# Kernel optimization log

Hardware: AMD Instinct MI355X
Metric: run time of the kernel (lower is better)

## Reference

```python
import math
import jax, jax.numpy as jnp
import numpy as np
from jax import lax

B, S, D = 2, 1024, 768
H, E, DH = 12, 8, 64          # n_head, num_experts, head dim
KA = 1                        # top-k experts per head (attention)
KF = 2                        # top-k experts per token (FFN)
DFF = 2048
EMA_DECAY = 0.99
CAP_FACTOR = 1.25
NEG_INF = -1e9


def setup_inputs() -> dict:
    key = jax.random.key(0)
    ks = jax.random.split(key, 16)
    sc = 0.02
    x = jax.random.normal(ks[0], (B, S, D), jnp.float32)
    causal = jnp.tril(jnp.ones((S, S), jnp.float32))
    mask = jnp.where(causal > 0, 0.0, NEG_INF).astype(jnp.float32)
    return {
        "x": x,
        "mask": mask,
        "W_q": jax.random.normal(ks[1], (D, D), jnp.float32) * sc,
        "W_k": jax.random.normal(ks[2], (D, D), jnp.float32) * sc,
        "W_v": jax.random.normal(ks[3], (H, E, DH, DH), jnp.float32) * sc,
        "W_o": jax.random.normal(ks[4], (H, E, DH, DH), jnp.float32) * sc,
        "W_router": jax.random.normal(ks[5], (D, H * E), jnp.float32) * sc,
        "g1": jnp.ones((D,), jnp.float32),
        "b1": jnp.zeros((D,), jnp.float32),
        "g2": jnp.ones((D,), jnp.float32),
        "b2": jnp.zeros((D,), jnp.float32),
        "gate_ff": jax.random.normal(ks[6], (D, E), jnp.float32) * sc,
        "W1": jax.random.normal(ks[7], (E, D, DFF), jnp.float32) * sc,
        "W2": jax.random.normal(ks[8], (E, DFF, D), jnp.float32) * sc,
    }


def layer_norm(x, g, b, eps=1e-5):
    m = jnp.mean(x, -1, keepdims=True)
    v = jnp.var(x, -1, keepdims=True)
    return (x - m) * lax.rsqrt(v + eps) * g + b


def head_switch_attention(x, mask, W_q, W_k, W_v, W_o, W_router):
    b, s, d = x.shape
    q = (x @ W_q).reshape(b, s, H, DH)
    k = (x @ W_k).reshape(b, s, H, DH)
    scores = jnp.einsum("bshd,bthd->bhst", q, k) / math.sqrt(DH) + mask
    p_attn = jax.nn.softmax(scores, axis=-1)          # (B,H,S,S)
    gate_logits = (x @ W_router).reshape(b, s, H, E)
    topk_scores, topk_idx = lax.top_k(gate_logits, KA)  # (B,S,H,KA)
    probs = jax.nn.softmax(topk_scores, axis=-1)
    x_h = x.reshape(b, s, H, DH)
    # value projections for all experts (small d_h x d_h GEMMs)
    v_all = jnp.einsum("bshd,hedf->bshef", x_h, W_v)
    y = jnp.zeros_like(x_h)
    hard_counts = jnp.zeros((H, E), jnp.float32)
    for slot in range(KA):
        oh = jax.nn.one_hot(topk_idx[..., slot], E, dtype=x.dtype)  # (B,S,H,E)
        v_sel = jnp.einsum("bshef,bshe->bshf", v_all, oh)
        # faithful to original einsum 'bhst,hbsd->hbtd' (sums over s)
        attn_out = jnp.einsum("bhst,bshf->bthf", p_attn, v_sel)
        o_all = jnp.einsum("bthf,hefg->btheg", attn_out, W_o)
        o_sel = jnp.einsum("btheg,bthe->bthg", o_all, oh)
        y = y + o_sel * probs[..., slot][..., None]
        hard_counts = hard_counts + lax.stop_gradient(oh).sum((0, 1))
    y = y.reshape(b, s, d)
    # EMA buffers start at zero -> ema = (1-decay)*hard/denom
    ema = hard_counts / (b * s * KA) * (1.0 - EMA_DECAY)
    p_lb = ema / (ema.sum() + 1e-9)
    aux = (p_lb * p_lb).sum() * E * H
    return y, aux


def moe_ffn(x, gate_ff, W1, W2):
    b, s, d = x.shape
    gate_logits = x @ gate_ff                      # (B,S,E), eval: no noise
    topk_scores, topk_idx = lax.top_k(gate_logits, KF)
    probs = jax.nn.softmax(topk_scores, axis=-1)   # (B,S,KF)
    capacity = math.ceil(CAP_FACTOR * (b * s) / E)
    flat_idx = topk_idx.reshape(-1)                # (B*S*KF,)
    oh_flat = jax.nn.one_hot(flat_idx, E, dtype=jnp.float32)
    tokens_so_far = jnp.cumsum(oh_flat, axis=0)
    keep = jnp.take_along_axis(tokens_so_far <= capacity, flat_idx[:, None], axis=1)[:, 0]
    probs = probs * keep.reshape(b, s, KF).astype(probs.dtype)
    probs = probs / (probs.sum(-1, keepdims=True) + 1e-9)
    oh = jax.nn.one_hot(topk_idx, E, dtype=probs.dtype)   # (B,S,KF,E)
    w = (probs[..., None] * oh).sum(2).reshape(b * s, E)  # combined weight per (token, expert)
    xf = x.reshape(b * s, d)
    yf = jnp.zeros_like(xf)
    for e in range(E):
        # scaling applied BEFORE ReLU, matching original x_sel = x * weight
        xe = xf * w[:, e:e + 1]
        yf = yf + jnp.maximum(xe @ W1[e], 0.0) @ W2[e]
    token_ctr = ((probs > 0)[..., None].astype(jnp.float32) * oh).sum((0, 1, 2))
    imp_ctr = (probs[..., None] * oh).sum((0, 1, 2))
    aux = ((token_ctr / token_ctr.sum()) * (imp_ctr / imp_ctr.sum())).sum() * E
    return yf.reshape(b, s, d), aux


def reference(x, mask, W_q, W_k, W_v, W_o, W_router, g1, b1, g2, b2, gate_ff, W1, W2):
    # pre-norm transformer block: x + Attn(LN(x)); x + MoEFFN(LN(x))
    a, aux1 = head_switch_attention(layer_norm(x, g1, b1), mask, W_q, W_k, W_v, W_o, W_router)
    x1 = x + a  # dropout is identity in eval
    f, aux2 = moe_ffn(layer_norm(x1, g2, b2), gate_ff, W1, W2)
    return x1 + f, aux1 + aux2
```

## Files before the change

kernel.cpp:

```cpp
#include <hip/hip_runtime.h>
#include <hip/hip_bf16.h>
#include <cstdint>

typedef __hip_bfloat16 bf16;
typedef __attribute__((ext_vector_type(8))) __bf16 bfrag;
typedef __attribute__((ext_vector_type(4))) float f32x4;

#define B_    2
#define S_    1024
#define D_    768
#define H_    12
#define E_    8
#define DH_   64
#define DFF_  2048
#define CAP_  320
#define CAPP_ 384
#define NTOK  (B_*S_)
#define NTH   (NTOK*H_)
#define QKLD  1536

__device__ __forceinline__ void stage16(const bf16* g, bf16* ldsLane){
#if __has_builtin(__builtin_amdgcn_global_load_lds)
  __builtin_amdgcn_global_load_lds((const __attribute__((address_space(1))) unsigned int*)g,
                                   (__attribute__((address_space(3))) unsigned int*)ldsLane, 16, 0, 0);
#else
  *(bfrag*)ldsLane = *(const bfrag*)g;
#endif
}

__global__ __launch_bounds__(256)
void transp_cvt(const float* __restrict__ src, bf16* __restrict__ dst,
                int K, int N, long sSrc, long sDst, int dstRowOff)
{
  src += (long)blockIdx.z*sSrc;
  dst += (long)blockIdx.z*sDst;
  __shared__ float t[32][33];
  int n0 = blockIdx.x*32, k0 = blockIdx.y*32;
  int tx = threadIdx.x & 31, ty = threadIdx.x >> 5;
#pragma unroll
  for (int r=0;r<4;r++){
    int kk = k0 + ty + r*8, nn = n0 + tx;
    t[ty+r*8][tx] = (nn < N) ? src[(long)kk*N + nn] : 0.f;
  }
  __syncthreads();
#pragma unroll
  for (int r=0;r<4;r++){
    int nn = n0 + ty + r*8;
    if (nn < N) dst[(long)(dstRowOff + nn)*K + k0 + tx] = __float2bfloat16(t[tx][ty+r*8]);
  }
}

__global__ __launch_bounds__(256)
void transp_f32(const float* __restrict__ src, float* __restrict__ dst, int K, int N)
{
  __shared__ float t[32][33];
  int n0 = blockIdx.x*32, k0 = blockIdx.y*32;
  int tx = threadIdx.x & 31, ty = threadIdx.x >> 5;
#pragma unroll
  for (int r=0;r<4;r++){
    int kk = k0 + ty + r*8, nn = n0 + tx;
    t[ty+r*8][tx] = (nn < N) ? src[(long)kk*N + nn] : 0.f;
  }
  __syncthreads();
#pragma unroll
  for (int r=0;r<4;r++){
    int nn = n0 + ty + r*8;
    if (nn < N) dst[(long)nn*K + k0 + tx] = t[tx][ty+r*8];
  }
}

__global__ __launch_bounds__(256)
void gemm_bn64(const bf16* __restrict__ A, const bf16* __restrict__ Bt,
               void* __restrict__ C, void* __restrict__ C2,
               int M, int N, int K, long sA, long sB, long sC, int relu, int outBf, int kSplit)
{
  int nwg = gridDim.x*gridDim.y*gridDim.z;
  int bid = blockIdx.x + gridDim.x*(blockIdx.y + gridDim.y*blockIdx.z);
  int nid = (bid & 7)*(nwg >> 3) + (bid >> 3);
  int bx = nid % gridDim.x;
  int t1 = nid / gridDim.x;
  int by = t1 % gridDim.y;
  int bz = t1 / gridDim.y;
  int e  = bz / kSplit, kc = bz - e*kSplit;
  A  += (long)e*sA;
  Bt += (long)e*sB;
  int kLen = K / kSplit, kBase = kc*kLen;
  int m0 = by*128, n0 = bx*64;
  __shared__ bf16 As[2][128*32];
  __shared__ bf16 Bs[2][64*32];
  int tid = threadIdx.x;
  int w = tid >> 6, lane = tid & 63;
  int quad = lane >> 4, l16 = lane & 15;
  int wm = w*32;
  f32x4 acc[2][4] = {};
  int srow = (lane >> 2);
  int gsw  = ((lane & 3) ^ (srow & 3))*8;
  const bf16* aBase = A + (long)m0*K;
  const bf16* bBase = Bt + (long)n0*K;
  int xr = (l16 & 3);
  int nIt = kLen >> 5;
  {
    int k0 = kBase;
#pragma unroll
    for (int j=0;j<2;j++){
      int c = w*2 + j, row = c*16 + srow;
      stage16(aBase + (long)row*K + k0 + gsw, As[0] + c*512 + lane*8);
    }
    int rowb = w*16 + srow;
    stage16(bBase + (long)rowb*K + k0 + gsw, Bs[0] + w*512 + lane*8);
  }
  int cur = 0;
  for (int it=0; it<nIt; ++it){
    __syncthreads();
    if (it+1 < nIt){
      int k0 = kBase + (it+1)*32;
      int nb = cur^1;
#pragma unroll
      for (int j=0;j<2;j++){
        int c = w*2 + j, row = c*16 + srow;
        stage16(aBase + (long)row*K + k0 + gsw, As[nb] + c*512 + lane*8);
      }
      int rowb = w*16 + srow;
      stage16(bBase + (long)rowb*K + k0 + gsw, Bs[nb] + w*512 + lane*8);
    }
    const bf16* Ac = As[cur];
    const bf16* Bc = Bs[cur];
    bfrag af[2], bfv[4];
#pragma unroll
    for (int t=0;t<2;t++) af[t]  = *(const bfrag*)(Ac + (wm + t*16 + l16)*32 + ((quad ^ xr)*8));
#pragma unroll
    for (int t=0;t<4;t++) bfv[t] = *(const bfrag*)(Bc + (t*16 + l16)*32 + ((quad ^ xr)*8));
#pragma unroll
    for (int ti=0;ti<2;ti++)
#pragma unroll
      for (int tj=0;tj<4;tj++)
        acc[ti][tj] = __builtin_amdgcn_mfma_f32_16x16x32_bf16(af[ti], bfv[tj], acc[ti][tj], 0, 0, 0);
    cur ^= 1;
  }
  long zoff = (long)e*sC;
  void* Cp = kc ? C2 : C;
  if (outBf){
    bf16* Cb = (bf16*)Cp + zoff;
#pragma unroll
    for (int ti=0;ti<2;ti++)
#pragma unroll
      for (int tj=0;tj<4;tj++)
#pragma unroll
        for (int r=0;r<4;r++){
          int row = m0 + wm + ti*16 + quad*4 + r;
          int col = n0 + tj*16 + l16;
          float v = acc[ti][tj][r];
          if (relu) v = fmaxf(v, 0.f);
          Cb[(long)row*N + col] = __float2bfloat16(v);
        }
  } else {
    float* Cf = (float*)Cp + zoff;
#pragma unroll
    for (int ti=0;ti<2;ti++)
#pragma unroll
      for (int tj=0;tj<4;tj++)
#pragma unroll
        for (int r=0;r<4;r++){
          int row = m0 + wm + ti*16 + quad*4 + r;
          int col = n0 + tj*16 + l16;
          float v = acc[ti][tj][r];
          if (relu) v = fmaxf(v, 0.f);
          Cf[(long)row*N + col] = v;
        }
  }
}

__global__ __launch_bounds__(256)
void ln_kernel(const float* __restrict__ src, const float* __restrict__ g, const float* __restrict__ bb,
               float* __restrict__ dstF, bf16* __restrict__ dstB,
               const float* __restrict__ gateW, float* __restrict__ glog2)
{
  int row = blockIdx.x, tid = threadIdx.x;
  __shared__ float red[256];
  __shared__ float gsum[4][E_];
  float v[3];
#pragma unroll
  for (int j=0;j<3;j++) v[j] = src[(long)row*D_ + tid + j*256];
  float s = v[0]+v[1]+v[2];
  red[tid]=s; __syncthreads();
  for (int o=128;o>0;o>>=1){ if(tid<o) red[tid]+=red[tid+o]; __syncthreads(); }
  float mean = red[0]*(1.0f/D_);
  __syncthreads();
  float sq = 0.f;
#pragma unroll
  for (int j=0;j<3;j++){ float d=v[j]-mean; sq += d*d; }
  red[tid]=sq; __syncthreads();
  for (int o=128;o>0;o>>=1){ if(tid<o) red[tid]+=red[tid+o]; __syncthreads(); }
  float rstd = rsqrtf(red[0]*(1.0f/D_) + 1e-5f);
  float ov[3];
#pragma unroll
  for (int j=0;j<3;j++){
    int d = tid + j*256;
    float o = (v[j]-mean)*rstd*g[d] + bb[d];
    ov[j] = o;
    dstF[(long)row*D_+d] = o;
    if (dstB) dstB[(long)row*D_+d] = __float2bfloat16(o);
  }
  if (gateW){
    float gp[E_] = {};
#pragma unroll
    for (int j=0;j<3;j++){
      int d = tid + j*256;
      const float* gw = gateW + (long)d*E_;
#pragma unroll
      for (int e=0;e<E_;e++) gp[e] += ov[j]*gw[e];
    }
#pragma unroll
    for (int off=1; off<64; off<<=1)
#pragma unroll
      for (int e=0;e<E_;e++) gp[e] += __shfl_xor(gp[e], off);
    if ((tid & 63) == 0)
#pragma unroll
      for (int e=0;e<E_;e++) gsum[tid>>6][e] = gp[e];
    __syncthreads();
    if (tid < E_)
      glog2[(long)row*E_ + tid] = gsum[0][tid]+gsum[1][tid]+gsum[2][tid]+gsum[3][tid];
  }
}

#define RTOK 4
__global__ __launch_bounds__(768)
void router_argmax(const float* __restrict__ ln1, const float* __restrict__ WrT,
                   int* __restrict__ eidx, int* __restrict__ gHist)
{
  int tok0 = blockIdx.x*RTOK;
  int tid = threadIdx.x;
  int col = tid >> 3, seg = tid & 7;
  __shared__ float xrow[RTOK][D_];
  __shared__ float logits[RTOK][96];
  for (int i=tid; i<RTOK*D_; i+=768){
    int t = i / D_, dpos = i - t*D_;
    xrow[t][dpos] = ln1[(long)(tok0+t)*D_ + dpos];
  }
  __syncthreads();
  const float* wrow = WrT + (long)col*D_;
  float acc[RTOK] = {};
#pragma unroll
  for (int j=0;j<24;j++){
    int dbase = j*32 + seg*4;
    float4 w = *(const float4*)(wrow + dbase);
#pragma unroll
    for (int t=0;t<RTOK;t++){
      float4 xv = *(const float4*)(&xrow[t][dbase]);
      acc[t] += xv.x*w.x + xv.y*w.y + xv.z*w.z + xv.w*w.w;
    }
  }
#pragma unroll
  for (int off=1; off<8; off<<=1)
#pragma unroll
    for (int t=0;t<RTOK;t++) acc[t] += __shfl_xor(acc[t], off);
  if (seg == 0)
#pragma unroll
    for (int t=0;t<RTOK;t++) logits[t][col] = acc[t];
  __syncthreads();
  if (tid < RTOK*H_){
    int t = tid / H_, h = tid % H_;
    const float* p = &logits[t][h*8];
    float best = p[0]; int bi = 0;
#pragma unroll
    for (int e=1;e<8;e++){ float v=p[e]; if (v > best){ best=v; bi=e; } }
    eidx[(tok0+t)*H_ + h] = bi;
    atomicAdd(&gHist[h*E_ + bi], 1);
  }
}

__global__ __launch_bounds__(64)
void vsel_kernel(const float* __restrict__ ln1, const float* __restrict__ Wv,
                 const int* __restrict__ eidx, bf16* __restrict__ vT)
{
  int blk = blockIdx.x;
  int h = blk % H_, tok = blk / H_;
  int b = tok >> 10, s = tok & 1023;
  int f = threadIdx.x;
  __shared__ float xs[DH_];
  xs[f] = ln1[(long)tok*D_ + h*DH_ + f];
  __syncthreads();
  int e = eidx[blk];
  const float* W = Wv + (long)(h*E_+e)*DH_*DH_;
  float acc = 0.f;
#pragma unroll 8
  for (int d=0; d<DH_; d++) acc += xs[d]*W[d*DH_ + f];
  vT[((long)(b*H_+h)*DH_ + f)*S_ + s] = __float2bfloat16(acc);
}

__global__ __launch_bounds__(256)
void attn_stats_mfma(const bf16* __restrict__ qkB, float* __restrict__ gM, float* __restrict__ gL)
{
  int s0 = blockIdx.x*64;
  int h = blockIdx.y, b = blockIdx.z;
  int tid = threadIdx.x;
  int w = tid >> 6, lane = tid & 63;
  int quad = lane >> 4, l16 = lane & 15;
  int x7 = l16 & 7;
  __shared__ bf16 ldsQ[64*64];
  __shared__ bf16 ldsK[2][64*64];
  const bf16* qbase = qkB + ((long)(b*S_ + s0))*QKLD + h*DH_;
  const bf16* kbase = qkB + ((long)(b*S_))*QKLD + 768 + h*DH_;
#pragma unroll
  for (int j=0;j<2;j++){
    int c = j*256 + tid;
    int row = c >> 3;
    int gs = ((c & 7) ^ (row & 7))*8;
    stage16(qbase + (long)row*QKLD + gs, ldsQ + c*8);
    stage16(kbase + (long)row*QKLD + gs, ldsK[0] + c*8);
  }
  float m_run[4] = {-1e30f,-1e30f,-1e30f,-1e30f};
  float l_run[4] = {0.f,0.f,0.f,0.f};
  int ttEnd = s0 >> 6;
  int cur = 0;
  for (int tt=0; tt<=ttEnd; tt++){
    __syncthreads();
    if (tt < ttEnd){
#pragma unroll
      for (int j=0;j<2;j++){
        int c = j*256 + tid;
        int row = c >> 3;
        int gs = ((c & 7) ^ (row & 7))*8;
        stage16(kbase + (long)((tt+1)*64 + row)*QKLD + gs, ldsK[cur^1] + c*8);
      }
    }
    const bf16* Kc = ldsK[cur];
    bfrag af0 = *(const bfrag*)(ldsQ + (w*16 + l16)*64 + ((quad     ^ x7)*8));
    bfrag af1 = *(const bfrag*)(ldsQ + (w*16 + l16)*64 + (((quad+4) ^ x7)*8));
    f32x4 cfr[4];
#pragma unroll
    for (int j=0;j<4;j++){
      bfrag b0 = *(const bfrag*)(Kc + (j*16 + l16)*64 + ((quad     ^ x7)*8));
      bfrag b1 = *(const bfrag*)(Kc + (j*16 + l16)*64 + (((quad+4) ^ x7)*8));
      f32x4 z = {};
      z = __builtin_amdgcn_mfma_f32_16x16x32_bf16(af0, b0, z, 0,0,0);
      z = __builtin_amdgcn_mfma_f32_16x16x32_bf16(af1, b1, z, 0,0,0);
      cfr[j] = z;
    }
#pragma unroll
    for (int r=0;r<4;r++){
      int s_g = s0 + w*16 + quad*4 + r;
      float v[4];
#pragma unroll
      for (int j=0;j<4;j++){
        int t_g = tt*64 + j*16 + l16;
        v[j] = (t_g <= s_g) ? cfr[j][r]*0.125f : -1e30f;
      }
      float mt = fmaxf(fmaxf(v[0],v[1]), fmaxf(v[2],v[3]));
#pragma unroll
      for (int mm=1; mm<16; mm<<=1) mt = fmaxf(mt, __shfl_xor(mt, mm));
      float mn = fmaxf(m_run[r], mt);
      float sum = __expf(v[0]-mn)+__expf(v[1]-mn)+__expf(v[2]-mn)+__expf(v[3]-mn);
#pragma unroll
      for (int mm=1; mm<16; mm<<=1) sum += __shfl_xor(sum, mm);
      l_run[r] = l_run[r]*__expf(m_run[r]-mn) + sum;
      m_run[r] = mn;
    }
    cur ^= 1;
  }
  if (l16 == 0){
    long base = ((long)(b*H_ + h))*S_ + s0 + w*16 + quad*4;
#pragma unroll
    for (int r=0;r<4;r++){ gM[base+r] = m_run[r]; gL[base+r] = l_run[r]; }
  }
}

__global__ __launch_bounds__(256)
void attn_pv(const bf16* __restrict__ qkB, const bf16* __restrict__ vT,
             const float* __restrict__ gM, const float* __restrict__ gL, float* __restrict__ aoH)
{
  int t0 = blockIdx.x*64;
  int h = blockIdx.y, b = blockIdx.z;
  int bh = b*H_ + h;
  int tid = threadIdx.x;
  int w = tid >> 6, lane = tid & 63;
  int quad = lane >> 4, l16 = lane & 15;
  int x7 = l16 & 7;
  __shared__ bf16 ldsK[64*64];
  __shared__ bf16 ldsQ[2][64*64];
  __shared__ bf16 ldsV[2][64*64];
  __shared__ bf16 ldsS[64*72];
  __shared__ float smx[2][64], sli[2][64];
  const bf16* kbase = qkB + ((long)(b*S_ + t0))*QKLD + 768 + h*DH_;
  const bf16* qbase = qkB + ((long)(b*S_))*QKLD + h*DH_;
  const bf16* vbase = vT + ((long)bh*DH_)*S_;
  int sb0 = t0 >> 6;
#pragma unroll
  for (int j=0;j<2;j++){
    int c = j*256 + tid;
    int row = c >> 3;
    int gs = ((c & 7) ^ (row & 7))*8;
    stage16(kbase + (long)row*QKLD + gs, ldsK + c*8);
    stage16(qbase + (long)(sb0*64 + row)*QKLD + gs, ldsQ[0] + c*8);
    stage16(vbase + (long)row*S_ + sb0*64 + gs, ldsV[0] + c*8);
  }
  if (tid < 64){
    smx[0][tid] = gM[(long)bh*S_ + sb0*64 + tid];
    sli[0][tid] = 1.0f / gL[(long)bh*S_ + sb0*64 + tid];
  }
  f32x4 accO[4] = {};
  int cur = 0;
  for (int sb = sb0; sb < S_/64; sb++){
    __syncthreads();
    if (sb+1 < S_/64){
      int nb = cur^1;
#pragma unroll
      for (int j=0;j<2;j++){
        int c = j*256 + tid;
        int row = c >> 3;
        int gs = ((c & 7) ^ (row & 7))*8;
        stage16(qbase + (long)((sb+1)*64 + row)*QKLD + gs, ldsQ[nb] + c*8);
        stage16(vbase + (long)row*S_ + (sb+1)*64 + gs, ldsV[nb] + c*8);
      }
      if (tid < 64){
        smx[nb][tid] = gM[(long)bh*S_ + (sb+1)*64 + tid];
        sli[nb][tid] = 1.0f / gL[(long)bh*S_ + (sb+1)*64 + tid];
      }
    }
    const bf16* Qc = ldsQ[cur];
    const bf16* Vc = ldsV[cur];
    bfrag af0 = *(const bfrag*)(ldsK + (w*16 + l16)*64 + ((quad     ^ x7)*8));
    bfrag af1 = *(const bfrag*)(ldsK + (w*16 + l16)*64 + (((quad+4) ^ x7)*8));
    f32x4 cs[4];
#pragma unroll
    for (int j=0;j<4;j++){
      bfrag b0 = *(const bfrag*)(Qc + (j*16 + l16)*64 + ((quad     ^ x7)*8));
      bfrag b1 = *(const bfrag*)(Qc + (j*16 + l16)*64 + (((quad+4) ^ x7)*8));
      f32x4 z = {};
      z = __builtin_amdgcn_mfma_f32_16x16x32_bf16(af0, b0, z, 0,0,0);
      z = __builtin_amdgcn_mfma_f32_16x16x32_bf16(af1, b1, z, 0,0,0);
      cs[j] = z;
    }
#pragma unroll
    for (int j=0;j<4;j++)
#pragma unroll
      for (int r=0;r<4;r++){
        int t_loc = w*16 + quad*4 + r;
        int s_loc = j*16 + l16;
        float wgt = ((t0 + t_loc) <= (sb*64 + s_loc))
                  ? __expf(cs[j][r]*0.125f - smx[cur][s_loc])*sli[cur][s_loc] : 0.f;
        ldsS[t_loc*72 + s_loc] = __float2bfloat16(wgt);
      }
    bfrag pa0 = *(const bfrag*)(ldsS + (w*16 + l16)*72 + quad*8);
    bfrag pa1 = *(const bfrag*)(ldsS + (w*16 + l16)*72 + 32 + quad*8);
#pragma unroll
    for (int j=0;j<4;j++){
      bfrag b0 = *(const bfrag*)(Vc + (j*16 + l16)*64 + ((quad     ^ x7)*8));
      bfrag b1 = *(const bfrag*)(Vc + (j*16 + l16)*64 + (((quad+4) ^ x7)*8));
      accO[j] = __builtin_amdgcn_mfma_f32_16x16x32_bf16(pa0, b0, accO[j], 0,0,0);
      accO[j] = __builtin_amdgcn_mfma_f32_16x16x32_bf16(pa1, b1, accO[j], 0,0,0);
    }
    cur ^= 1;
  }
#pragma unroll
  for (int j=0;j<4;j++)
#pragma unroll
    for (int r=0;r<4;r++){
      int t_loc = w*16 + quad*4 + r;
      int f = j*16 + l16;
      aoH[((long)bh*S_ + t0 + t_loc)*DH_ + f] = accO[j][r];
    }
}

__global__ __launch_bounds__(64)
void oproj_kernel(const float* __restrict__ aoH, const float* __restrict__ Wo,
                  const int* __restrict__ eidx, const float* __restrict__ x,
                  float* __restrict__ x1)
{
  int blk = blockIdx.x;
  int h = blk % H_, tok = blk / H_;
  int b = tok >> 10, s = tok & 1023;
  int g = threadIdx.x;
  __shared__ float xs[DH_];
  xs[g] = aoH[((long)(b*H_+h)*S_ + s)*DH_ + g];
  __syncthreads();
  int e = eidx[blk];
  const float* W = Wo + (long)(h*E_+e)*DH_*DH_;
  float acc = 0.f;
#pragma unroll 8
  for (int f=0; f<DH_; f++) acc += xs[f]*W[f*DH_ + g];
  long idx = (long)tok*D_ + h*DH_ + g;
  x1[idx] = x[idx] + acc;
}

__global__ __launch_bounds__(256)
void route_kernel(const float* __restrict__ glog2, const int* __restrict__ gHist,
                  int* __restrict__ gI0, int* __restrict__ gI1,
                  int* __restrict__ gPos0, int* __restrict__ gPos1,
                  int* __restrict__ listTok, float* __restrict__ listW,
                  int* __restrict__ gCnt, float* __restrict__ auxOut)
{
  __shared__ unsigned char sI0[NTOK], sI1[NTOK];
  __shared__ float sP0[NTOK], sP1[NTOK];
  __shared__ short sPos0[NTOK], sPos1[NTOK];
  __shared__ int   sScan[256*E_];
  __shared__ int   sHist[H_*E_];
  __shared__ float sImp[E_];
  __shared__ int   sCnt[E_];
  int tid = threadIdx.x;
  if (tid < E_) sImp[tid] = 0.f;
  if (tid < H_*E_) sHist[tid] = gHist[tid];
  for (int i=tid; i<NTOK; i+=256){
    const float* p = glog2 + (long)i*E_;
    float b0 = p[0]; int e0 = 0;
#pragma unroll
    for (int e=1;e<E_;e++){ float vv=p[e]; if (vv > b0){ b0=vv; e0=e; } }
    float b1v = -1e30f; int e1 = 0;
#pragma unroll
    for (int e=0;e<E_;e++){ if (e==e0) continue; float vv=p[e]; if (vv > b1v){ b1v=vv; e1=e; } }
    float ex = __expf(b1v - b0);
    float inv = 1.f/(1.f + ex);
    sI0[i] = (unsigned char)e0; sI1[i] = (unsigned char)e1;
    sP0[i] = inv; sP1[i] = ex*inv;
    gI0[i] = e0; gI1[i] = e1;
  }
  __syncthreads();
  {
    int myCnt[E_] = {};
#pragma unroll
    for (int j=0;j<16;j++){
      int i = tid*16 + j;
      int tok = i >> 1;
      int e = (i & 1) ? (int)sI1[tok] : (int)sI0[tok];
      myCnt[e]++;
    }
#pragma unroll
    for (int e=0;e<E_;e++) sScan[tid*E_+e] = myCnt[e];
    __syncthreads();
    for (int off=1; off<256; off<<=1){
      int v[E_];
      if (tid >= off){
#pragma unroll
        for (int e=0;e<E_;e++) v[e] = sScan[(tid-off)*E_+e];
      }
      __syncthreads();
      if (tid >= off){
#pragma unroll
        for (int e=0;e<E_;e++) sScan[tid*E_+e] += v[e];
      }
      __syncthreads();
    }
    int pref[E_];
#pragma unroll
    for (int e=0;e<E_;e++) pref[e] = tid ? sScan[(tid-1)*E_+e] : 0;
#pragma unroll
    for (int j=0;j<16;j++){
      int i = tid*16 + j;
      int tok = i >> 1;
      int e = (i & 1) ? (int)sI1[tok] : (int)sI0[tok];
      int pos = pref[e]++;
      short p = (pos < CAP_) ? (short)pos : (short)-1;
      if (i & 1) sPos1[tok] = p; else sPos0[tok] = p;
    }
    if (tid < E_){
      int cnt = sScan[255*E_ + tid];
      sCnt[tid] = cnt < CAP_ ? cnt : CAP_;
      gCnt[tid] = sCnt[tid];
    }
  }
  __syncthreads();
  for (int i=tid; i<NTOK; i+=256){
    int e0 = sI0[i], e1 = sI1[i];
    int p0i = sPos0[i], p1i = sPos1[i];
    float k0 = p0i >= 0 ? 1.f : 0.f, k1 = p1i >= 0 ? 1.f : 0.f;
    float p0 = sP0[i], p1 = sP1[i];
    float denom = p0*k0 + p1*k1 + 1e-9f;
    float w0 = p0*k0/denom, w1 = p1*k1/denom;
    if (p0i >= 0){ listTok[e0*CAP_+p0i] = i; listW[e0*CAP_+p0i] = w0; atomicAdd(&sImp[e0], w0); }
    if (p1i >= 0){ listTok[e1*CAP_+p1i] = i; listW[e1*CAP_+p1i] = w1; atomicAdd(&sImp[e1], w1); }
    gPos0[i] = p0i; gPos1[i] = p1i;
  }
  __syncthreads();
  if (tid == 0){
    float tot = 0.f;
    for (int i=0;i<H_*E_;i++) tot += (float)sHist[i]*(1.0f/NTOK)*0.01f;
    float a1 = 0.f;
    for (int i=0;i<H_*E_;i++){
      float p = ((float)sHist[i]*(1.0f/NTOK)*0.01f)/(tot + 1e-9f);
      a1 += p*p;
    }
    a1 *= (float)(H_*E_);
    float tcs = 0.f, ims = 0.f;
    for (int e=0;e<E_;e++){ tcs += (float)sCnt[e]; ims += sImp[e]; }
    float a2 = 0.f;
    for (int e=0;e<E_;e++) a2 += ((float)sCnt[e]/tcs)*(sImp[e]/ims);
    a2 *= (float)E_;
    auxOut[0] = a1 + a2;
  }
}

__global__ __launch_bounds__(256)
void gather_kernel(const float* __restrict__ ln2, const int* __restrict__ listTok,
                   const float* __restrict__ listW, const int* __restrict__ gCnt,
                   bf16* __restrict__ Xg)
{
  int blk = blockIdx.x;
  int e = blk / CAPP_, r = blk % CAPP_;
  int tid = threadIdx.x;
  bool live = r < gCnt[e];
  int tok = 0; float w = 0.f;
  if (live){ tok = listTok[e*CAP_+r]; w = listW[e*CAP_+r]; }
  for (int d=tid; d<D_; d+=256)
    Xg[(long)blk*D_ + d] = __float2bfloat16(live ? ln2[(long)tok*D_+d]*w : 0.f);
}

__global__ __launch_bounds__(256)
void combine_kernel(const float* __restrict__ x1,
                    const float* __restrict__ Ya, const float* __restrict__ Yb,
                    const int* __restrict__ gI0, const int* __restrict__ gI1,
                    const int* __restrict__ gPos0, const int* __restrict__ gPos1,
                    float* __restrict__ out)
{
  int i = blockIdx.x;
  int tid = threadIdx.x;
  int p0 = gPos0[i], p1 = gPos1[i];
  int e0 = gI0[i],  e1 = gI1[i];
  long off0 = (long)(e0*CAPP_ + (p0 >= 0 ? p0 : 0))*D_;
  long off1 = (long)(e1*CAPP_ + (p1 >= 0 ? p1 : 0))*D_;
  const float* y0a = Ya + off0; const float* y0b = Yb + off0;
  const float* y1a = Ya + off1; const float* y1b = Yb + off1;
  for (int d=tid; d<D_; d+=256){
    float v = x1[(long)i*D_+d];
    if (p0 >= 0) v += y0a[d] + y0b[d];
    if (p1 >= 0) v += y1a[d] + y1b[d];
    out[(long)i*D_+d] = v;
  }
}

extern "C" void kernel_launch(void* const* d_in, const int* in_sizes, int n_in,
                              void* d_out, int out_size, void* d_ws, size_t ws_size,
                              hipStream_t stream)
{
  const float* x    = (const float*)d_in[0];
  const float* W_q  = (const float*)d_in[2];
  const float* W_k  = (const float*)d_in[3];
  const float* W_v  = (const float*)d_in[4];
  const float* W_o  = (const float*)d_in[5];
  const float* W_r  = (const float*)d_in[6];
  const float* g1   = (const float*)d_in[7];
  const float* b1   = (const float*)d_in[8];
  const float* g2   = (const float*)d_in[9];
  const float* b2   = (const float*)d_in[10];
  const float* gate = (const float*)d_in[11];
  const float* W1   = (const float*)d_in[12];
  const float* W2   = (const float*)d_in[13];
  float* out = (float*)d_out;

  float* wsf = (float*)d_ws;
  const long oX1   = 0;
  const long oLnF  = 1572864;
  const long oLnB  = 3145728;
  const long oWcat = 3932160;
  const long oWrT  = 4521984;
  const long oHist = 4595712;
  const long oGM   = 4718592;
  const long oGL   = 4743168;
  const long oEidx = 4767744;
  const long oGlg2 = 4792320;
  const long oI0   = 4808704;
  const long oI1   = 4810752;
  const long oP0   = 4812800;
  const long oP1   = 4814848;
  const long oLT   = 4816896;
  const long oLW   = 4819456;
  const long oCnt  = 4822016;
  const long SB    = 4822528;
  const long TOTAL = SB + 12976128;
  if (ws_size < (size_t)TOTAL*4) return;

  float* x1    = wsf + oX1;
  float* lnbF  = wsf + oLnF;
  bf16*  lnbB  = (bf16*)(wsf + oLnB);
  bf16*  WcatB = (bf16*)(wsf + oWcat);
  float* WrT   = wsf + oWrT;
  int*   gHist = (int*)(wsf + oHist);
  float* gM    = wsf + oGM;
  float* gL    = wsf + oGL;
  int*   eidx  = (int*)(wsf + oEidx);
  float* glog2 = wsf + oGlg2;
  int*   gI0   = (int*)(wsf + oI0);
  int*   gI1   = (int*)(wsf + oI1);
  int*   gPos0 = (int*)(wsf + oP0);
  int*   gPos1 = (int*)(wsf + oP1);
  int*   lTok  = (int*)(wsf + oLT);
  float* lW    = wsf + oLW;
  int*   gCnt  = (int*)(wsf + oCnt);
  bf16*  qkB   = (bf16*)(wsf + SB);
  bf16*  vT    = (bf16*)(wsf + SB + 1572864);
  float* aoH   = wsf + SB + 2359296;
  bf16*  WT    = (bf16*)(wsf + SB);
  bf16*  Xg    = (bf16*)(wsf + SB + 6291456);
  bf16*  Hid   = (bf16*)(wsf + SB + 7471104);
  float* Yexp  = wsf + SB + 10616832;
  float* YexpB = wsf + oLnF;

  hipMemsetAsync(gHist, 0, H_*E_*sizeof(int), stream);
  transp_cvt<<<dim3(24,24,1),256,0,stream>>>(W_q, WcatB, 768, 768, 0, 0, 0);
  transp_cvt<<<dim3(24,24,1),256,0,stream>>>(W_k, WcatB, 768, 768, 0, 0, 768);
  transp_f32<<<dim3(3,24,1),256,0,stream>>>(W_r, WrT, 768, 96);

  ln_kernel<<<NTOK,256,0,stream>>>(x, g1, b1, lnbF, lnbB, nullptr, nullptr);
  gemm_bn64<<<dim3(24,16,1),256,0,stream>>>(lnbB, WcatB, qkB, nullptr, 2048, QKLD, 768, 0,0,0, 0, 1, 1);
  router_argmax<<<NTOK/RTOK,768,0,stream>>>(lnbF, WrT, eidx, gHist);
  vsel_kernel<<<NTH,64,0,stream>>>(lnbF, W_v, eidx, vT);
  attn_stats_mfma<<<dim3(S_/64,H_,B_),256,0,stream>>>(qkB, gM, gL);
  attn_pv<<<dim3(S_/64,H_,B_),256,0,stream>>>(qkB, vT, gM, gL, aoH);
  oproj_kernel<<<NTH,64,0,stream>>>(aoH, W_o, eidx, x, x1);

  ln_kernel<<<NTOK,256,0,stream>>>(x1, g2, b2, lnbF, nullptr, gate, glog2);
  route_kernel<<<1,256,0,stream>>>(glog2, gHist, gI0,gI1,gPos0,gPos1, lTok,lW,gCnt, out + (size_t)NTOK*D_);
  gather_kernel<<<E_*CAPP_,256,0,stream>>>(lnbF, lTok, lW, gCnt, Xg);
  transp_cvt<<<dim3(64,24,8),256,0,stream>>>(W1, WT, 768, 2048, (long)768*2048, (long)2048*768, 0);
  gemm_bn64<<<dim3(32,3,8),256,0,stream>>>(Xg, WT, Hid, nullptr, CAPP_, DFF_, 768,
                                           (long)CAPP_*768, (long)2048*768, (long)CAPP_*2048, 1, 1, 1);
  transp_cvt<<<dim3(24,64,8),256,0,stream>>>(W2, WT, 2048, 768, (long)2048*768, (long)768*2048, 0);
  gemm_bn64<<<dim3(12,3,16),256,0,stream>>>(Hid, WT, Yexp, YexpB, CAPP_, 768, 2048,
                                            (long)CAPP_*2048, (long)768*2048, (long)CAPP_*768, 0, 0, 2);
  combine_kernel<<<NTOK,256,0,stream>>>(x1, Yexp, YexpB, gI0,gI1,gPos0,gPos1, out);
}
```

Baseline: 417.3 us.

## Group tokens by head-expert for V and O projections with LDS-cached weights

The router now builds per-(head,expert) token lists with atomics, and the per-token V-select and O-projection kernels are replaced by blocks that each load one 64x64 expert weight into LDS and process all tokens routed to it. This removes repeated global weight reads across 24K tiny single-wave blocks. The attention-stats kernel also defers the cross-lane max/sum reductions until after the key loop, and the two Q/K weight transposes are merged into one launch. In exchange it adds an extra memset, atomics for list building, and nondeterministic token order within each list, plus possible load imbalance across experts.

```diff
diff --git a/kernel.cpp b/kernel.cpp
--- a/kernel.cpp
+++ b/kernel.cpp
@@ -18,6 +18,7 @@
 #define NTOK  (B_*S_)
 #define NTH   (NTOK*H_)
 #define QKLD  1536
+#define NHE   (H_*E_)
 
 __device__ __forceinline__ void stage16(const bf16* g, bf16* ldsLane){
 #if __has_builtin(__builtin_amdgcn_global_load_lds)
@@ -26,6 +27,23 @@
 #else
   *(bfrag*)ldsLane = *(const bfrag*)g;
 #endif
+}
+
+__global__ __launch_bounds__(256)
+void transp_qk(const float* __restrict__ Wq, const float* __restrict__ Wk, bf16* __restrict__ dst)
+{
+  const float* src = blockIdx.z ? Wk : Wq;
+  int rowOff = blockIdx.z ? 768 : 0;
+  __shared__ float t[32][33];
+  int n0 = blockIdx.x*32, k0 = blockIdx.y*32;
+  int tx = threadIdx.x & 31, ty = threadIdx.x >> 5;
+#pragma unroll
+  for (int r=0;r<4;r++)
+    t[ty+r*8][tx] = src[(long)(k0 + ty + r*8)*D_ + n0 + tx];
+  __syncthreads();
+#pragma unroll
+  for (int r=0;r<4;r++)
+    dst[(long)(rowOff + n0 + ty + r*8)*D_ + k0 + tx] = __float2bfloat16(t[tx][ty+r*8]);
 }
 
 __global__ __launch_bounds__(256)
@@ -226,7 +244,8 @@
 #define RTOK 4
 __global__ __launch_bounds__(768)
 void router_argmax(const float* __restrict__ ln1, const float* __restrict__ WrT,
-                   int* __restrict__ eidx, int* __restrict__ gHist)
+                   int* __restrict__ eidx, int* __restrict__ gHist,
+                   int* __restrict__ hCnt, int* __restrict__ hList)
 {
   int tok0 = blockIdx.x*RTOK;
   int tid = threadIdx.x;
@@ -264,28 +283,40 @@
     float best = p[0]; int bi = 0;
 #pragma unroll
     for (int e=1;e<8;e++){ float v=p[e]; if (v > best){ best=v; bi=e; } }
-    eidx[(tok0+t)*H_ + h] = bi;
+    int tok = tok0 + t;
+    eidx[tok*H_ + h] = bi;
     atomicAdd(&gHist[h*E_ + bi], 1);
-  }
-}
-
-__global__ __launch_bounds__(64)
-void vsel_kernel(const float* __restrict__ ln1, const float* __restrict__ Wv,
-                 const int* __restrict__ eidx, bf16* __restrict__ vT)
-{
-  int blk = blockIdx.x;
-  int h = blk % H_, tok = blk / H_;
-  int b = tok >> 10, s = tok & 1023;
-  int f = threadIdx.x;
-  __shared__ float xs[DH_];
-  xs[f] = ln1[(long)tok*D_ + h*DH_ + f];
-  __syncthreads();
-  int e = eidx[blk];
-  const float* W = Wv + (long)(h*E_+e)*DH_*DH_;
-  float acc = 0.f;
+    int he = h*E_ + bi;
+    int pos = atomicAdd(&hCnt[he], 1);
+    hList[he*NTOK + pos] = tok;
+  }
+}
+
+__global__ __launch_bounds__(256)
+void vsel_b(const float* __restrict__ ln1, const float* __restrict__ Wv,
+            const int* __restrict__ hCnt, const int* __restrict__ hList,
+            bf16* __restrict__ vT)
+{
+  int he = blockIdx.x;
+  int h = he >> 3;
+  __shared__ float Ws[DH_*DH_];
+  __shared__ float xsh[4][DH_];
+  int tid = threadIdx.x;
+  const float* W = Wv + (long)he*DH_*DH_;
+  for (int i=tid; i<DH_*DH_; i+=256) Ws[i] = W[i];
+  int cnt = hCnt[he];
+  __syncthreads();
+  int w = tid >> 6, lane = tid & 63;
+  const int* lst = hList + (long)he*NTOK;
+  for (int i = blockIdx.y*4 + w; i < cnt; i += 32){
+    int tok = lst[i];
+    int b = tok >> 10, s = tok & 1023;
+    xsh[w][lane] = ln1[(long)tok*D_ + h*DH_ + lane];
+    float acc = 0.f;
 #pragma unroll 8
-  for (int d=0; d<DH_; d++) acc += xs[d]*W[d*DH_ + f];
-  vT[((long)(b*H_+h)*DH_ + f)*S_ + s] = __float2bfloat16(acc);
+    for (int d=0; d<DH_; d++) acc += xsh[w][d]*Ws[d*DH_ + lane];
+    vT[((long)(b*H_+h)*DH_ + lane)*S_ + s] = __float2bfloat16(acc);
+  }
 }
 
 __global__ __launch_bounds__(256)
@@ -309,8 +340,8 @@
     stage16(qbase + (long)row*QKLD + gs, ldsQ + c*8);
     stage16(kbase + (long)row*QKLD + gs, ldsK[0] + c*8);
   }
-  float m_run[4] = {-1e30f,-1e30f,-1e30f,-1e30f};
-  float l_run[4] = {0.f,0.f,0.f,0.f};
+  float m_ln[4] = {-1e30f,-1e30f,-1e30f,-1e30f};
+  float l_ln[4] = {0.f,0.f,0.f,0.f};
   int ttEnd = s0 >> 6;
   int cur = 0;
   for (int tt=0; tt<=ttEnd; tt++){
@@ -340,23 +371,28 @@
 #pragma unroll
     for (int r=0;r<4;r++){
       int s_g = s0 + w*16 + quad*4 + r;
-      float v[4];
-#pragma unroll
-      for (int j=0;j<4;j++){
-        int t_g = tt*64 + j*16 + l16;
-        v[j] = (t_g <= s_g) ? cfr[j][r]*0.125f : -1e30f;
-      }
-      float mt = fmaxf(fmaxf(v[0],v[1]), fmaxf(v[2],v[3]));
-#pragma unroll
-      for (int mm=1; mm<16; mm<<=1) mt = fmaxf(mt, __shfl_xor(mt, mm));
-      float mn = fmaxf(m_run[r], mt);
-      float sum = __expf(v[0]-mn)+__expf(v[1]-mn)+__expf(v[2]-mn)+__expf(v[3]-mn);
-#pragma unroll
-      for (int mm=1; mm<16; mm<<=1) sum += __shfl_xor(sum, mm);
-      l_run[r] = l_run[r]*__expf(m_run[r]-mn) + sum;
-      m_run[r] = mn;
+      float v0 = (tt*64      + l16 <= s_g) ? cfr[0][r]*0.125f : -1e30f;
+      float v1 = (tt*64 + 16 + l16 <= s_g) ? cfr[1][r]*0.125f : -1e30f;
+      float v2 = (tt*64 + 32 + l16 <= s_g) ? cfr[2][r]*0.125f : -1e30f;
+      float v3 = (tt*64 + 48 + l16 <= s_g) ? cfr[3][r]*0.125f : -1e30f;
+      float mt = fmaxf(fmaxf(v0,v1), fmaxf(v2,v3));
+      float mn = fmaxf(m_ln[r], mt);
+      l_ln[r] = l_ln[r]*__expf(m_ln[r]-mn)
+              + ((__expf(v0-mn)+__expf(v1-mn)) + (__expf(v2-mn)+__expf(v3-mn)));
+      m_ln[r] = mn;
     }
     cur ^= 1;
+  }
+  float m_run[4], l_run[4];
+#pragma unroll
+  for (int r=0;r<4;r++){
+    float mf = m_ln[r];
+#pragma unroll
+    for (int mm=1; mm<16; mm<<=1) mf = fmaxf(mf, __shfl_xor(mf, mm));
+    float lf = l_ln[r]*__expf(m_ln[r]-mf);
+#pragma unroll
+    for (int mm=1; mm<16; mm<<=1) lf += __shfl_xor(lf, mm);
+    m_run[r] = mf; l_run[r] = lf;
   }
   if (l16 == 0){
     long base = ((long)(b*H_ + h))*S_ + s0 + w*16 + quad*4;
@@ -462,25 +498,32 @@
     }
 }
 
-__global__ __launch_bounds__(64)
-void oproj_kernel(const float* __restrict__ aoH, const float* __restrict__ Wo,
-                  const int* __restrict__ eidx, const float* __restrict__ x,
-                  float* __restrict__ x1)
-{
-  int blk = blockIdx.x;
-  int h = blk % H_, tok = blk / H_;
-  int b = tok >> 10, s = tok & 1023;
-  int g = threadIdx.x;
-  __shared__ float xs[DH_];
-  xs[g] = aoH[((long)(b*H_+h)*S_ + s)*DH_ + g];
-  __syncthreads();
-  int e = eidx[blk];
-  const float* W = Wo + (long)(h*E_+e)*DH_*DH_;
-  float acc = 0.f;
+__global__ __launch_bounds__(256)
+void oproj_b(const float* __restrict__ aoH, const float* __restrict__ Wo,
+             const int* __restrict__ hCnt, const int* __restrict__ hList,
+             const float* __restrict__ x, float* __restrict__ x1)
+{
+  int he = blockIdx.x;
+  int h = he >> 3;
+  __shared__ float Ws[DH_*DH_];
+  __shared__ float xsh[4][DH_];
+  int tid = threadIdx.x;
+  const float* W = Wo + (long)he*DH_*DH_;
+  for (int i=tid; i<DH_*DH_; i+=256) Ws[i] = W[i];
+  int cnt = hCnt[he];
+  __syncthreads();
+  int w = tid >> 6, lane = tid & 63;
+  const int* lst = hList + (long)he*NTOK;
+  for (int i = blockIdx.y*4 + w; i < cnt; i += 32){
+    int tok = lst[i];
+    int b = tok >> 10, s = tok & 1023;
+    xsh[w][lane] = aoH[((long)(b*H_+h)*S_ + s)*DH_ + lane];
+    float acc = 0.f;
 #pragma unroll 8
-  for (int f=0; f<DH_; f++) acc += xs[f]*W[f*DH_ + g];
-  long idx = (long)tok*D_ + h*DH_ + g;
-  x1[idx] = x[idx] + acc;
+    for (int f=0; f<DH_; f++) acc += xsh[w][f]*Ws[f*DH_ + lane];
+    long idx = (long)tok*D_ + h*DH_ + lane;
+    x1[idx] = x[idx] + acc;
+  }
 }
 
 __global__ __launch_bounds__(256)
@@ -664,6 +707,7 @@
   const long oLT   = 4816896;
   const long oLW   = 4819456;
   const long oCnt  = 4822016;
+  const long oHCnt = 4822100;
   const long SB    = 4822528;
   const long TOTAL = SB + 12976128;
   if (ws_size < (size_t)TOTAL*4) return;
@@ -685,9 +729,11 @@
   int*   lTok  = (int*)(wsf + oLT);
   float* lW    = wsf + oLW;
   int*   gCnt  = (int*)(wsf + oCnt);
+  int*   hCnt  = (int*)(wsf + oHCnt);
   bf16*  qkB   = (bf16*)(wsf + SB);
   bf16*  vT    = (bf16*)(wsf + SB + 1572864);
   float* aoH   = wsf + SB + 2359296;
+  int*   hList = (int*)(wsf + SB + 3932160);
   bf16*  WT    = (bf16*)(wsf + SB);
   bf16*  Xg    = (bf16*)(wsf + SB + 6291456);
   bf16*  Hid   = (bf16*)(wsf + SB + 7471104);
@@ -695,17 +741,17 @@
   float* YexpB = wsf + oLnF;
 
   hipMemsetAsync(gHist, 0, H_*E_*sizeof(int), stream);
-  transp_cvt<<<dim3(24,24,1),256,0,stream>>>(W_q, WcatB, 768, 768, 0, 0, 0);
-  transp_cvt<<<dim3(24,24,1),256,0,stream>>>(W_k, WcatB, 768, 768, 0, 0, 768);
+  hipMemsetAsync(hCnt, 0, NHE*sizeof(int), stream);
+  transp_qk<<<dim3(24,24,2),256,0,stream>>>(W_q, W_k, WcatB);
   transp_f32<<<dim3(3,24,1),256,0,stream>>>(W_r, WrT, 768, 96);
 
   ln_kernel<<<NTOK,256,0,stream>>>(x, g1, b1, lnbF, lnbB, nullptr, nullptr);
   gemm_bn64<<<dim3(24,16,1),256,0,stream>>>(lnbB, WcatB, qkB, nullptr, 2048, QKLD, 768, 0,0,0, 0, 1, 1);
-  router_argmax<<<NTOK/RTOK,768,0,stream>>>(lnbF, WrT, eidx, gHist);
-  vsel_kernel<<<NTH,64,0,stream>>>(lnbF, W_v, eidx, vT);
+  router_argmax<<<NTOK/RTOK,768,0,stream>>>(lnbF, WrT, eidx, gHist, hCnt, hList);
+  vsel_b<<<dim3(NHE,8,1),256,0,stream>>>(lnbF, W_v, hCnt, hList, vT);
   attn_stats_mfma<<<dim3(S_/64,H_,B_),256,0,stream>>>(qkB, gM, gL);
   attn_pv<<<dim3(S_/64,H_,B_),256,0,stream>>>(qkB, vT, gM, gL, aoH);
-  oproj_kernel<<<NTH,64,0,stream>>>(aoH, W_o, eidx, x, x1);
+  oproj_b<<<dim3(NHE,8,1),256,0,stream>>>(aoH, W_o, hCnt, hList, x, x1);
 
   ln_kernel<<<NTOK,256,0,stream>>>(x1, g2, b2, lnbF, nullptr, gate, glog2);
   route_kernel<<<1,256,0,stream>>>(glog2, gHist, gI0,gI1,gPos0,gPos1, lTok,lW,gCnt, out + (size_t)NTOK*D_);
```

New measurement: 405.6 us. -2.8%, faster.
